# Kernel tuning notes

Hardware: AMD Instinct MI355X
Metric: run time of the kernel (lower is better)

The kernel has to match this reference:

```python
import jax, jax.numpy as jnp
import numpy as np

DIM = 1536
NH = 12
HD = 128
EPS = 1e-6


def _rope(x, freqs, f, h, w, start):
    # x: [B,S,N,D] with S == f*h*w; freqs: [1024, D//2, 2] (real, imag) unit rotations
    B, S, N, D = x.shape
    c = D // 2
    c0 = c - 2 * (c // 3)
    c1 = c // 3
    ff = jnp.broadcast_to(freqs[start:start + f, :c0][:, None, None], (f, h, w, c0, 2))
    fh = jnp.broadcast_to(freqs[:h, c0:c0 + c1][None, :, None], (f, h, w, c1, 2))
    fw = jnp.broadcast_to(freqs[:w, c0 + c1:c][None, None, :], (f, h, w, c1, 2))
    fr = jnp.concatenate([ff, fh, fw], axis=3).reshape(S, 1, c, 2)  # [S,1,c,2]
    xr, xi = x[..., 0::2], x[..., 1::2]          # interleaved real/imag pairs
    cr, ci = fr[None, ..., 0], fr[None, ..., 1]  # [1,S,1,c]
    yr = xr * cr - xi * ci
    yi = xr * ci + xi * cr
    return jnp.stack([yr, yi], axis=-1).reshape(B, S, N, D)


def _rms(x, g):
    return x * jax.lax.rsqrt(jnp.mean(x * x, axis=-1, keepdims=True) + EPS) * g


def setup_inputs():
    key = jax.random.key(0)
    ks = jax.random.split(key, 16)
    S = 3 * 30 * 52  # chunk_size = 3 frames * 1560 tokens/frame
    x = jax.random.normal(ks[0], (1, S, DIM), jnp.float32)
    fr = jax.random.normal(ks[1], (1024, HD // 2, 2), jnp.float32)
    fr = fr / jnp.sqrt(jnp.sum(fr * fr, axis=-1, keepdims=True) + 1e-12)  # unit-modulus rotations
    g_kmean = jax.random.uniform(ks[2], (1, NH, HD), jnp.float32)  # mean of relu(k): nonnegative
    g_kv = jax.random.normal(ks[3], (1, NH, HD, HD), jnp.float32) * 0.05
    p = lambda i, shp: jax.random.normal(ks[i], shp, jnp.float32) * 0.02
    return dict(
        x=x, freqs=fr, g_kmean=g_kmean, g_kv=g_kv,
        Wq=p(4, (DIM, DIM)), bq=p(5, (DIM,)),
        Wk=p(6, (DIM, DIM)), bk=p(7, (DIM,)),
        Wv=p(8, (DIM, DIM)), bv=p(9, (DIM,)),
        Wo=p(10, (DIM, DIM)), bo=p(11, (DIM,)),
        gq=jnp.ones((DIM,), jnp.float32), gk=jnp.ones((DIM,), jnp.float32),
        Wlin=p(12, (HD, HD)), blin=p(13, (HD,)),
        f_frames=3, h_grid=30, w_grid=52,
    )


def reference(x, freqs, g_kmean, g_kv, Wq, bq, Wk, bk, Wv, bv, Wo, bo, gq, gk, Wlin, blin, f_frames, h_grid, w_grid):
    B, S, _ = x.shape
    q = _rms(x @ Wq.T + bq, gq).reshape(B, S, NH, HD)
    k = _rms(x @ Wk.T + bk, gk).reshape(B, S, NH, HD)
    v = (x @ Wv.T + bv).reshape(B, S, NH, HD)
    rq = _rope(q, freqs, f_frames, h_grid, w_grid, 0)
    rk = _rope(k, freqs, f_frames, h_grid, w_grid, 0)
    # local window attention: at step 0 (current_start=0, empty cache, sink_size=0)
    # the working kv window is exactly the roped current chunk
    scores = jnp.einsum('bsnd,btnd->bnst', rq, rk) * (HD ** -0.5)
    x_local = jnp.einsum('bnst,btnd->bsnd', jax.nn.softmax(scores, axis=-1), v)
    # global linear-attention branch (kernel_func = relu feature map on q, roped q against kv state)
    qf = jax.nn.relu(q)
    z = 1.0 / (jnp.einsum('bsnd,bnd->bsn', qf, g_kmean) + 1e-6)
    xg = jnp.einsum('bsnd,bndm->bsnm', rq, g_kv) * z[..., None]
    xg = xg @ Wlin.T + blin
    out = (x_local + xg).reshape(B, S, DIM) @ Wo.T + bo
    return out
```

## Files before the change

kernel.cpp:

```cpp
#include <hip/hip_runtime.h>

typedef short s16x8 __attribute__((ext_vector_type(8)));
typedef float f32x4 __attribute__((ext_vector_type(4)));
typedef float f32x16 __attribute__((ext_vector_type(16)));
typedef unsigned short u16x4 __attribute__((ext_vector_type(4)));
typedef unsigned int u32x4 __attribute__((ext_vector_type(4)));

#define QSCALE (0.08838834764831845f * 1.4426950408889634f)

__device__ __forceinline__ unsigned short f2bf(float f) {
  unsigned int u = __float_as_uint(f);
  u += 0x7fffu + ((u >> 16) & 1u);
  return (unsigned short)(u >> 16);
}
__device__ __forceinline__ float bf2f(unsigned short h) {
  return __uint_as_float((unsigned int)h << 16);
}
__device__ __forceinline__ float fast_exp2(float x) {
  float r;
  asm("v_exp_f32 %0, %1" : "=v"(r) : "v"(x));
  return r;
}

__device__ __forceinline__ void gload16(const void* gp, void* lp) {
  __builtin_amdgcn_global_load_lds(
      (const __attribute__((address_space(1))) void*)gp,
      (__attribute__((address_space(3))) void*)lp,
      16, 0, 0);
}

__global__ void cast_f32_bf16_x4(const float* __restrict__ in,
                                 unsigned short* __restrict__ out, int n4) {
  int i = blockIdx.x * 256 + threadIdx.x;
  if (i >= n4) return;
  f32x4 v = *((const f32x4*)in + i);
  u16x4 o;
  o[0] = f2bf(v[0]); o[1] = f2bf(v[1]); o[2] = f2bf(v[2]); o[3] = f2bf(v[3]);
  *((u16x4*)out + i) = o;
}

__global__ void g2fill_kernel(const float* __restrict__ g_kv,
                              const float* __restrict__ Wlin,
                              unsigned short* __restrict__ G2c) {
  int h = blockIdx.x, m = blockIdx.y, d = threadIdx.x;
  const float* gk = g_kv + ((size_t)h * 128 + d) * 128;
  const float* wl = Wlin + (size_t)m * 128;
  float s = 0.f;
  for (int j = 0; j < 128; ++j) s += gk[j] * wl[j];
  G2c[((size_t)h * 128 + m) * 128 + d] = f2bf(s * (1.0f / QSCALE));
}

template <int MODE>
__global__ __launch_bounds__(256) void gemm_bt(
    const unsigned short* __restrict__ A, const unsigned short* __restrict__ B,
    const float* __restrict__ bias, void* __restrict__ Cout,
    int M, int N, int K, int lda, int ldb,
    const float* __restrict__ o0buf, const float* __restrict__ zbuf,
    const float* __restrict__ o1buf, const float* __restrict__ lbuf, int nsplit) {
  __shared__ __align__(16) unsigned short Asm_[128 * 64];
  __shared__ __align__(16) unsigned short Bsm_[128 * 64];
  const int tid = threadIdx.x;
  const int wid = tid >> 6, lane = tid & 63;
  const int mt = blockIdx.x, nt = blockIdx.y;
  const int wr = wid >> 1, wc = wid & 1;
  const int acol = (MODE == 3) ? nt * 128 : 0;
  f32x4 acc[4][4] = {};

  const int st_srccol = ((((lane & 7) << 4) ^ ((lane >> 3) << 4)) >> 1);
  const int st_rowoff = (lane >> 3);

  for (int k0 = 0; k0 < K; k0 += 64) {
    __syncthreads();
#pragma unroll
    for (int r = 0; r < 4; ++r) {
      int c = wid * 4 + r;
      int lrow = c * 8 + st_rowoff;
      int arow = mt * 128 + lrow; if (arow > M - 1) arow = M - 1;
      gload16(A + (size_t)arow * lda + acol + k0 + st_srccol,
              (char*)Asm_ + c * 1024 + lane * 16);
      int brow = nt * 128 + lrow;
      gload16(B + (size_t)brow * ldb + k0 + st_srccol,
              (char*)Bsm_ + c * 1024 + lane * 16);
    }
    __syncthreads();
#pragma unroll
    for (int kk = 0; kk < 2; ++kk) {
      int cb = (kk * 64 + ((lane >> 4) << 4)) ^ ((lane & 7) << 4);
      s16x8 af[4], bfr[4];
#pragma unroll
      for (int m = 0; m < 4; ++m)
        af[m] = *(const s16x8*)((const char*)Asm_ + (wr * 64 + m * 16 + (lane & 15)) * 128 + cb);
#pragma unroll
      for (int n = 0; n < 4; ++n)
        bfr[n] = *(const s16x8*)((const char*)Bsm_ + (wc * 64 + n * 16 + (lane & 15)) * 128 + cb);
#pragma unroll
      for (int m = 0; m < 4; ++m)
#pragma unroll
        for (int n = 0; n < 4; ++n)
          acc[m][n] = __builtin_amdgcn_mfma_f32_16x16x32_bf16(af[m], bfr[n], acc[m][n], 0, 0, 0);
    }
  }
  const int rb = mt * 128 + wr * 64, cbse = nt * 128 + wc * 64;
#pragma unroll
  for (int m = 0; m < 4; ++m) {
#pragma unroll
    for (int n = 0; n < 4; ++n) {
#pragma unroll
      for (int rg = 0; rg < 4; ++rg) {
        int rr = rb + m * 16 + ((lane >> 4) << 2) + rg;
        int cc = cbse + n * 16 + (lane & 15);
        if (rr < M) {
          float v = acc[m][n][rg];
          if (MODE == 0) {
            v += bias[cc];
            ((unsigned short*)Cout)[(size_t)rr * N + cc] = f2bf(v);
          } else if (MODE == 1) {
            v += bias[cc];
            ((float*)Cout)[(size_t)rr * N + cc] = v;
          } else {
            int hd = cc >> 7;
            float lsum = lbuf[(size_t)rr * 12 + hd];
            float osum = o0buf[(size_t)rr * N + cc];
            for (int s = 1; s < nsplit; ++s) {
              lsum += lbuf[((size_t)s * M + rr) * 12 + hd];
              osum += o1buf[(size_t)(s - 1) * M * 1536 + (size_t)rr * N + cc];
            }
            v = v * zbuf[(size_t)rr * 12 + hd] + osum * (1.0f / lsum) + bias[cc & 127];
            ((unsigned short*)Cout)[(size_t)rr * N + cc] = f2bf(v);
          }
        }
      }
    }
  }
}

__global__ __launch_bounds__(256) void rms_rope_kernel(
    const unsigned short* __restrict__ pre, const float* __restrict__ freqs,
    const float* __restrict__ g, const float* __restrict__ g_kmean,
    unsigned short* __restrict__ outr, float* __restrict__ zout,
    int S, int ld, float oscale,
    const int* __restrict__ hgp, const int* __restrict__ wgp) {
  const int s = blockIdx.x;
  const int tid = threadIdx.x;
  const int lane = tid & 63, wid = tid >> 6;
  const unsigned short* row = pre + (size_t)s * ld;
  unsigned int pv0, pv1, pv2;
  float ssq = 0.f;
  {
    pv0 = *(const unsigned int*)(row + 2 * (tid));
    pv1 = *(const unsigned int*)(row + 2 * (tid + 256));
    pv2 = *(const unsigned int*)(row + 2 * (tid + 512));
    float a0 = bf2f((unsigned short)(pv0 & 0xffffu)), b0 = bf2f((unsigned short)(pv0 >> 16));
    float a1 = bf2f((unsigned short)(pv1 & 0xffffu)), b1 = bf2f((unsigned short)(pv1 >> 16));
    float a2 = bf2f((unsigned short)(pv2 & 0xffffu)), b2 = bf2f((unsigned short)(pv2 >> 16));
    ssq = a0 * a0 + b0 * b0 + a1 * a1 + b1 * b1 + a2 * a2 + b2 * b2;
  }
#pragma unroll
  for (int m = 1; m < 64; m <<= 1) ssq += __shfl_xor(ssq, m, 64);
  __shared__ float wpart[4];
  if (lane == 0) wpart[wid] = ssq;
  __syncthreads();
  float tot = wpart[0] + wpart[1] + wpart[2] + wpart[3];
  float rms = rsqrtf(tot * (1.0f / 1536.0f) + 1e-6f);
  const int Wg = *wgp;
  const int HWg = (*hgp) * Wg;
  int fi = s / HWg; int rem = s - fi * HWg;
  int hi = rem / Wg; int wi = rem - hi * Wg;
  unsigned int pvs[3] = {pv0, pv1, pv2};
#pragma unroll
  for (int rd = 0; rd < 3; ++rd) {
    int p = tid + rd * 256;
    int c = p & 63;
    int fidx = (c < 22) ? fi : ((c < 43) ? hi : wi);
    float cr = freqs[fidx * 128 + 2 * c];
    float ci = freqs[fidx * 128 + 2 * c + 1];
    float xr = bf2f((unsigned short)(pvs[rd] & 0xffffu)) * rms * g[2 * p];
    float xi = bf2f((unsigned short)(pvs[rd] >> 16)) * rms * g[2 * p + 1];
    float yr = (xr * cr - xi * ci) * oscale;
    float yi = (xr * ci + xi * cr) * oscale;
    unsigned int ow = (unsigned int)f2bf(yr) | ((unsigned int)f2bf(yi) << 16);
    *(unsigned int*)(outr + (size_t)s * 1536 + 2 * p) = ow;
    if (zout != nullptr) {
      int head = p >> 6;
      float part = fmaxf(xr, 0.f) * g_kmean[head * 128 + 2 * c] +
                   fmaxf(xi, 0.f) * g_kmean[head * 128 + 2 * c + 1];
#pragma unroll
      for (int m = 1; m < 64; m <<= 1) part += __shfl_xor(part, m, 64);
      if (lane == 0) zout[(size_t)s * 12 + head] = 1.0f / (part + 1e-6f);
    }
  }
}

__global__ __launch_bounds__(256) void vtrans_kernel(const unsigned short* __restrict__ vpre,
                                                     unsigned short* __restrict__ vt, int S, int ld) {
  __shared__ unsigned short tile[64][66];
  int t0 = blockIdx.x * 64, c0 = blockIdx.y * 64;
  int tid = threadIdx.x;
#pragma unroll
  for (int rep = 0; rep < 16; ++rep) {
    int lin = rep * 256 + tid;
    int i = lin >> 6, j = lin & 63;
    int t = t0 + i; if (t > S - 1) t = S - 1;
    tile[i][j] = vpre[(size_t)t * ld + c0 + j];
  }
  __syncthreads();
#pragma unroll
  for (int rep = 0; rep < 16; ++rep) {
    int lin = rep * 256 + tid;
    int j = lin >> 6, i = lin & 63;
    int t = t0 + i;
    if (t < S) vt[(size_t)(c0 + j) * S + t] = tile[i][j];
  }
}

__global__ __launch_bounds__(256, 3) void attn_kernel(
    const unsigned short* __restrict__ rq, const unsigned short* __restrict__ rk,
    const unsigned short* __restrict__ vt, float* __restrict__ o0buf,
    float* __restrict__ o1buf, float* __restrict__ lbuf, int S, int nqb, int nsplit) {
  __shared__ __align__(16) unsigned short Ks[2][32 * 128];
  __shared__ __align__(16) unsigned short Vs[2][128 * 32];
  const int tid = threadIdx.x, wid = tid >> 6, lane = tid & 63;
  const int q32 = lane & 31, hi = lane >> 5;

  const int total = nqb * 12 * nsplit;
  int lg = blockIdx.x;
  if ((total & 7) == 0) lg = (lg & 7) * (total >> 3) + (lg >> 3);
  const int z = lg / (nqb * 12);
  int rem = lg - z * nqb * 12;
  const int h = rem / nqb;
  const int qb = rem - h * nqb;
  const int q0 = qb * 128 + wid * 32;

  const int seg = (((S + nsplit - 1) / nsplit) + 31) & ~31;
  const int tbeg = z * seg;
  const int tend = (tbeg + seg < S) ? (tbeg + seg) : S;
  float* obufz = (z == 0) ? o0buf : (o1buf + (size_t)(z - 1) * S * 1536);
  float* lbufz = lbuf + (size_t)z * S * 12;

  s16x8 qf[8];
  {
    int qrow = q0 + q32; if (qrow > S - 1) qrow = S - 1;
    const unsigned short* qp = rq + (size_t)qrow * 1536 + h * 128 + hi * 8;
#pragma unroll
    for (int dblk = 0; dblk < 8; ++dblk) qf[dblk] = *(const s16x8*)(qp + dblk * 16);
  }
  f32x16 o0 = {}, o1 = {}, o2 = {}, o3 = {};
  float lsum = 0.f;

  const int k_tok0 = tid >> 4;
  const int k_off = (tid & 15) * 16;
  const int v_d0 = tid >> 2;
  const int v_toff = (tid & 3) * 16;
  const int vswz = ((q32 >> 1) & 3) << 4;

#define STAGE(buf, t0s)                                                            \
  {                                                                                \
    _Pragma("unroll") for (int r = 0; r < 2; ++r) {                                \
      int ktok = k_tok0 + 16 * r;                                                  \
      int kb = k_off ^ ((ktok & 7) << 4);                                          \
      int trow = (t0s) + ktok; if (trow > S - 1) trow = S - 1;                     \
      gload16(rk + (size_t)trow * 1536 + h * 128 + (kb >> 1),                      \
              (char*)Ks[buf] + r * 4096 + tid * 16);                               \
      int dd = v_d0 + 64 * r;                                                      \
      int vb_ = v_toff ^ (((dd >> 1) & 3) << 4);                                   \
      int vtok = (t0s) + (vb_ >> 1); if (vtok > S - 8) vtok = S - 8;               \
      gload16(vt + (size_t)(h * 128 + dd) * S + vtok,                              \
              (char*)Vs[buf] + r * 4096 + tid * 16);                               \
    }                                                                              \
  }

  STAGE(0, tbeg);
  __syncthreads();
  int cur = 0;
  for (int t0 = tbeg; t0 < tend; t0 += 32) {
    if (t0 + 32 < tend) STAGE(cur ^ 1, t0 + 32);
    f32x16 sc = {};
    __builtin_amdgcn_s_setprio(1);
#pragma unroll
    for (int dblk = 0; dblk < 8; ++dblk) {
      s16x8 kfr = *(const s16x8*)((const char*)Ks[cur] + q32 * 256 +
                                  ((dblk * 32 + hi * 16) ^ ((q32 & 7) << 4)));
      sc = __builtin_amdgcn_mfma_f32_32x32x16_bf16(kfr, qf[dblk], sc, 0, 0, 0);
    }
    __builtin_amdgcn_s_setprio(0);
    const bool full = (t0 + 32 <= tend);
    unsigned int pk[8];
    float rs = 0.f;
#pragma unroll
    for (int j = 0; j < 8; ++j) {
      float p0, p1;
      if (full) {
        p0 = fast_exp2(sc[2 * j]);
        p1 = fast_exp2(sc[2 * j + 1]);
      } else {
        int r0 = 2 * j;
        int tk0 = t0 + (r0 & 3) + 8 * (r0 >> 2) + 4 * hi;
        p0 = (tk0 < tend) ? fast_exp2(sc[2 * j]) : 0.f;
        p1 = (tk0 + 1 < tend) ? fast_exp2(sc[2 * j + 1]) : 0.f;
      }
      unsigned int u0 = __float_as_uint(p0) & 0xffff0000u;
      unsigned int u1 = __float_as_uint(p1) & 0xffff0000u;
      rs += __uint_as_float(u0) + __uint_as_float(u1);
      pk[j] = (u0 >> 16) | u1;
    }
    lsum += rs;
    unsigned int x0 = pk[0], y0 = pk[2], x1 = pk[1], y1 = pk[3];
    asm("v_permlane32_swap_b32 %0, %1" : "+v"(x0), "+v"(y0));
    asm("v_permlane32_swap_b32 %0, %1" : "+v"(x1), "+v"(y1));
    unsigned int x2 = pk[4], y2 = pk[6], x3 = pk[5], y3 = pk[7];
    asm("v_permlane32_swap_b32 %0, %1" : "+v"(x2), "+v"(y2));
    asm("v_permlane32_swap_b32 %0, %1" : "+v"(x3), "+v"(y3));
    u32x4 pa0v = {x0, x1, y0, y1};
    u32x4 pa1v = {x2, x3, y2, y3};
    s16x8 pa0 = __builtin_bit_cast(s16x8, pa0v);
    s16x8 pa1 = __builtin_bit_cast(s16x8, pa1v);
    __builtin_amdgcn_s_setprio(1);
#pragma unroll
    for (int ks = 0; ks < 2; ++ks) {
      s16x8 pa = ks ? pa1 : pa0;
      const int tb = (ks * 32 + hi * 16) ^ vswz;
      const char* vbase = (const char*)Vs[cur] + q32 * 64 + tb;
      s16x8 vb;
      vb = *(const s16x8*)(vbase + 0 * 2048);
      o0 = __builtin_amdgcn_mfma_f32_32x32x16_bf16(pa, vb, o0, 0, 0, 0);
      vb = *(const s16x8*)(vbase + 1 * 2048);
      o1 = __builtin_amdgcn_mfma_f32_32x32x16_bf16(pa, vb, o1, 0, 0, 0);
      vb = *(const s16x8*)(vbase + 2 * 2048);
      o2 = __builtin_amdgcn_mfma_f32_32x32x16_bf16(pa, vb, o2, 0, 0, 0);
      vb = *(const s16x8*)(vbase + 3 * 2048);
      o3 = __builtin_amdgcn_mfma_f32_32x32x16_bf16(pa, vb, o3, 0, 0, 0);
    }
    __builtin_amdgcn_s_setprio(0);
    __syncthreads();
    cur ^= 1;
  }
  lsum += __shfl_xor(lsum, 32, 64);
  {
    int qrow = q0 + q32;
    if (hi == 0 && qrow < S) lbufz[(size_t)qrow * 12 + h] = lsum;
  }
#pragma unroll
  for (int r = 0; r < 16; ++r) {
    int qrow = q0 + (r & 3) + 8 * (r >> 2) + 4 * hi;
    if (qrow < S) {
      float* orow = obufz + (size_t)qrow * 1536 + h * 128 + q32;
      orow[0] = o0[r]; orow[32] = o1[r]; orow[64] = o2[r]; orow[96] = o3[r];
    }
  }
#undef STAGE
}

extern "C" void kernel_launch(void* const* d_in, const int* in_sizes, int n_in,
                              void* d_out, int out_size, void* d_ws, size_t ws_size,
                              hipStream_t stream) {
  const float* x = (const float*)d_in[0];
  const float* freqs = (const float*)d_in[1];
  const float* g_kmean = (const float*)d_in[2];
  const float* g_kv = (const float*)d_in[3];
  const float* Wq = (const float*)d_in[4];  const float* bq = (const float*)d_in[5];
  const float* Wk = (const float*)d_in[6];  const float* bk = (const float*)d_in[7];
  const float* Wv = (const float*)d_in[8];  const float* bv = (const float*)d_in[9];
  const float* Wo = (const float*)d_in[10]; const float* bo = (const float*)d_in[11];
  const float* gq = (const float*)d_in[12]; const float* gk = (const float*)d_in[13];
  const float* Wlin = (const float*)d_in[14]; const float* blin = (const float*)d_in[15];
  const int* hgp = (const int*)d_in[17];
  const int* wgp = (const int*)d_in[18];

  const int S = in_sizes[0] / 1536;

  char* ws = (char*)d_ws;
  const size_t SZ = (size_t)S * 1536 * 2;
  const size_t OSZ = (size_t)S * 1536 * 4;
  const size_t WSZ = (size_t)1536 * 1536 * 2;
  const size_t QKVSZ = (size_t)S * 4608 * 2;
  const size_t G2SZ = (size_t)12 * 128 * 128 * 2;
  size_t o_xbf = 0;
  size_t o_wqkv = o_xbf + SZ;
  size_t o_wo = o_wqkv + 3 * WSZ;
  size_t o_g2 = o_wo + WSZ;
  size_t o_qkv = o_g2 + G2SZ;
  size_t o_rk = o_qkv + QKVSZ;
  size_t o_vt = o_rk + SZ;
  size_t o_z = o_vt + SZ;
  size_t o_bqkv = o_z + (size_t)S * 12 * 4;
  size_t o_o1 = o_bqkv + 4608 * 4;

  int nsplit = 4;
  if (ws_size < o_o1 + (size_t)3 * OSZ + (size_t)4 * S * 12 * 4) nsplit = 2;
  size_t o_l = o_o1 + (size_t)(nsplit - 1) * OSZ;
  size_t need = o_l + (size_t)nsplit * S * 12 * 4;
  if (ws_size < need) return;

  unsigned short* xbf = (unsigned short*)(ws + o_xbf);
  unsigned short* wqkv = (unsigned short*)(ws + o_wqkv);
  unsigned short* wob = (unsigned short*)(ws + o_wo);
  unsigned short* g2c = (unsigned short*)(ws + o_g2);
  unsigned short* qkv = (unsigned short*)(ws + o_qkv);
  unsigned short* rkb = (unsigned short*)(ws + o_rk);
  unsigned short* vtb = (unsigned short*)(ws + o_vt);
  float* zbuf = (float*)(ws + o_z);
  float* bqkv = (float*)(ws + o_bqkv);
  unsigned short* rqb = xbf;
  float* o0buf = (float*)(ws + o_qkv);
  float* o1buf = (float*)(ws + o_o1);
  float* lbuf = (float*)(ws + o_l);
  unsigned short* ybf = (unsigned short*)(ws + o_qkv + OSZ);

  {
    int n4 = (S * 1536) / 4;
    cast_f32_bf16_x4<<<(n4 + 255) / 256, 256, 0, stream>>>(x, xbf, n4);
    int w4 = (1536 * 1536) / 4;
    int wg = (w4 + 255) / 256;
    cast_f32_bf16_x4<<<wg, 256, 0, stream>>>(Wq, wqkv, w4);
    cast_f32_bf16_x4<<<wg, 256, 0, stream>>>(Wk, wqkv + (size_t)1536 * 1536, w4);
    cast_f32_bf16_x4<<<wg, 256, 0, stream>>>(Wv, wqkv + (size_t)2 * 1536 * 1536, w4);
    cast_f32_bf16_x4<<<wg, 256, 0, stream>>>(Wo, wob, w4);
  }
  hipMemcpyAsync(bqkv, bq, 1536 * 4, hipMemcpyDeviceToDevice, stream);
  hipMemcpyAsync(bqkv + 1536, bk, 1536 * 4, hipMemcpyDeviceToDevice, stream);
  hipMemcpyAsync(bqkv + 3072, bv, 1536 * 4, hipMemcpyDeviceToDevice, stream);

  g2fill_kernel<<<dim3(12, 128), 128, 0, stream>>>(g_kv, Wlin, g2c);

  {
    dim3 ggrid((S + 127) / 128, 36);
    gemm_bt<0><<<ggrid, 256, 0, stream>>>(xbf, wqkv, bqkv, qkv, S, 4608, 1536, 1536, 1536,
                                          nullptr, nullptr, nullptr, nullptr, 0);
  }

  rms_rope_kernel<<<S, 256, 0, stream>>>(qkv, freqs, gq, g_kmean, rqb, zbuf, S, 4608, QSCALE, hgp, wgp);
  rms_rope_kernel<<<S, 256, 0, stream>>>(qkv + 1536, freqs, gk, nullptr, rkb, nullptr, S, 4608, 1.0f, hgp, wgp);

  vtrans_kernel<<<dim3((S + 63) / 64, 24), 256, 0, stream>>>(qkv + 3072, vtb, S, 4608);

  {
    int nqb = (S + 127) / 128;
    attn_kernel<<<dim3(nqb * 12 * nsplit), 256, 0, stream>>>(rqb, rkb, vtb,
                                                             o0buf, o1buf, lbuf, S, nqb, nsplit);
  }

  {
    dim3 ggrid((S + 127) / 128, 12);
    gemm_bt<3><<<ggrid, 256, 0, stream>>>(rqb, g2c, blin, ybf, S, 1536, 128, 1536, 128,
                                          o0buf, zbuf, o1buf, lbuf, nsplit);
    gemm_bt<1><<<ggrid, 256, 0, stream>>>(ybf, wob, bo, (float*)d_out, S, 1536, 1536, 1536, 1536,
                                          nullptr, nullptr, nullptr, nullptr, 0);
  }
}
```

Before: 464.5 us.

## Triple-buffer K/V staging in attention and fix KV split count to two

The attention kernel's K/V shared-memory staging goes from a double buffer to a ring of three, prefetching two tiles ahead. Each iteration now waits with explicit vmcnt counts and a raw s_barrier instead of __syncthreads, so one tile's loads can stay in flight across the barrier. The KV split count is also fixed at 2 instead of 4, which halves the partial-output buffers and combine work but gives fewer, longer blocks. Shared memory per block grows from 32 KB to 48 KB, which may lower occupancy relative to the launch bound of 3 blocks.

```diff
diff --git a/kernel.cpp b/kernel.cpp
--- a/kernel.cpp
+++ b/kernel.cpp
@@ -217,8 +217,8 @@
     const unsigned short* __restrict__ rq, const unsigned short* __restrict__ rk,
     const unsigned short* __restrict__ vt, float* __restrict__ o0buf,
     float* __restrict__ o1buf, float* __restrict__ lbuf, int S, int nqb, int nsplit) {
-  __shared__ __align__(16) unsigned short Ks[2][32 * 128];
-  __shared__ __align__(16) unsigned short Vs[2][128 * 32];
+  __shared__ __align__(16) unsigned short Ks[3 * 32 * 128];
+  __shared__ __align__(16) unsigned short Vs[3 * 32 * 128];
   const int tid = threadIdx.x, wid = tid >> 6, lane = tid & 63;
   const int q32 = lane & 31, hi = lane >> 5;
 
@@ -260,25 +260,38 @@
       int kb = k_off ^ ((ktok & 7) << 4);                                          \
       int trow = (t0s) + ktok; if (trow > S - 1) trow = S - 1;                     \
       gload16(rk + (size_t)trow * 1536 + h * 128 + (kb >> 1),                      \
-              (char*)Ks[buf] + r * 4096 + tid * 16);                               \
+              (char*)Ks + (buf) * 8192 + r * 4096 + tid * 16);                     \
       int dd = v_d0 + 64 * r;                                                      \
       int vb_ = v_toff ^ (((dd >> 1) & 3) << 4);                                   \
       int vtok = (t0s) + (vb_ >> 1); if (vtok > S - 8) vtok = S - 8;               \
       gload16(vt + (size_t)(h * 128 + dd) * S + vtok,                              \
-              (char*)Vs[buf] + r * 4096 + tid * 16);                               \
+              (char*)Vs + (buf) * 8192 + r * 4096 + tid * 16);                     \
     }                                                                              \
   }
 
   STAGE(0, tbeg);
-  __syncthreads();
+  if (tbeg + 32 < tend) {
+    STAGE(1, tbeg + 32);
+    asm volatile("s_waitcnt vmcnt(4)" ::: "memory");
+  } else {
+    asm volatile("s_waitcnt vmcnt(0)" ::: "memory");
+  }
+  __builtin_amdgcn_sched_barrier(0);
+  __builtin_amdgcn_s_barrier();
+  __builtin_amdgcn_sched_barrier(0);
+
   int cur = 0;
   for (int t0 = tbeg; t0 < tend; t0 += 32) {
-    if (t0 + 32 < tend) STAGE(cur ^ 1, t0 + 32);
+    const bool staged = (t0 + 64 < tend);
+    int stg = cur + 2; if (stg >= 3) stg -= 3;
+    if (staged) STAGE(stg, t0 + 64);
+    const char* Kc = (const char*)Ks + cur * 8192;
+    const char* Vc = (const char*)Vs + cur * 8192;
     f32x16 sc = {};
     __builtin_amdgcn_s_setprio(1);
 #pragma unroll
     for (int dblk = 0; dblk < 8; ++dblk) {
-      s16x8 kfr = *(const s16x8*)((const char*)Ks[cur] + q32 * 256 +
+      s16x8 kfr = *(const s16x8*)(Kc + q32 * 256 +
                                   ((dblk * 32 + hi * 16) ^ ((q32 & 7) << 4)));
       sc = __builtin_amdgcn_mfma_f32_32x32x16_bf16(kfr, qf[dblk], sc, 0, 0, 0);
     }
@@ -319,7 +332,7 @@
     for (int ks = 0; ks < 2; ++ks) {
       s16x8 pa = ks ? pa1 : pa0;
       const int tb = (ks * 32 + hi * 16) ^ vswz;
-      const char* vbase = (const char*)Vs[cur] + q32 * 64 + tb;
+      const char* vbase = Vc + q32 * 64 + tb;
       s16x8 vb;
       vb = *(const s16x8*)(vbase + 0 * 2048);
       o0 = __builtin_amdgcn_mfma_f32_32x32x16_bf16(pa, vb, o0, 0, 0, 0);
@@ -331,8 +344,15 @@
       o3 = __builtin_amdgcn_mfma_f32_32x32x16_bf16(pa, vb, o3, 0, 0, 0);
     }
     __builtin_amdgcn_s_setprio(0);
-    __syncthreads();
-    cur ^= 1;
+    if (staged) {
+      asm volatile("s_waitcnt vmcnt(4)" ::: "memory");
+    } else {
+      asm volatile("s_waitcnt vmcnt(0)" ::: "memory");
+    }
+    __builtin_amdgcn_sched_barrier(0);
+    __builtin_amdgcn_s_barrier();
+    __builtin_amdgcn_sched_barrier(0);
+    cur = cur + 1; if (cur >= 3) cur = 0;
   }
   lsum += __shfl_xor(lsum, 32, 64);
   {
@@ -367,6 +387,7 @@
   const int* wgp = (const int*)d_in[18];
 
   const int S = in_sizes[0] / 1536;
+  const int nsplit = 2;
 
   char* ws = (char*)d_ws;
   const size_t SZ = (size_t)S * 1536 * 2;
@@ -384,9 +405,6 @@
   size_t o_z = o_vt + SZ;
   size_t o_bqkv = o_z + (size_t)S * 12 * 4;
   size_t o_o1 = o_bqkv + 4608 * 4;
-
-  int nsplit = 4;
-  if (ws_size < o_o1 + (size_t)3 * OSZ + (size_t)4 * S * 12 * 4) nsplit = 2;
   size_t o_l = o_o1 + (size_t)(nsplit - 1) * OSZ;
   size_t need = o_l + (size_t)nsplit * S * 12 * 4;
   if (ws_size < need) return;
```

Result: no change. 461.7 us (-0.6%).

## Replace QKV GEMM with 256x256-tile double-buffered 8-wave kernel

Applied to the files above, without the earlier changes.

Adds a new bf16 GEMM kernel using 256x256 output tiles, 512 threads, double-buffered swizzled LDS staging interleaved with MFMA phases and setprio, and uses it for the fused QKV projection. The bigger tile raises data reuse per block and overlaps global loads with compute, cutting the global traffic and LDS stalls of the 128x128 kernel. It also pins the attention split count to 2 instead of choosing 4 when workspace allows, which changes attention occupancy and the number of partial buffers to combine. The grid for S=4680 holds only 19x18 blocks, so wave quantisation and the single-block-per-CU launch bound are risks.

```diff
diff --git a/kernel.cpp b/kernel.cpp
--- a/kernel.cpp
+++ b/kernel.cpp
@@ -48,6 +48,133 @@
   float s = 0.f;
   for (int j = 0; j < 128; ++j) s += gk[j] * wl[j];
   G2c[((size_t)h * 128 + m) * 128 + d] = f2bf(s * (1.0f / QSCALE));
+}
+
+__global__ __launch_bounds__(512, 1) void gemm256_bt(
+    const unsigned short* __restrict__ A, const unsigned short* __restrict__ B,
+    const float* __restrict__ bias, unsigned short* __restrict__ C,
+    int M, int N, int K) {
+  __shared__ __align__(16) unsigned short lds[2 * 2 * 2 * 128 * 64];
+  const int tid = threadIdx.x;
+  const int lane = tid & 63;
+  const int wid = tid >> 6;
+  const int wr = wid >> 2, wc = wid & 3;
+  const int mt = blockIdx.x, nt = blockIdx.y;
+
+  f32x4 acc[8][4] = {};
+
+  int st_row[2], st_col[2];
+#pragma unroll
+  for (int rep = 0; rep < 2; ++rep) {
+    int D = (rep * 512 + tid) * 16;
+    int L = D ^ (((D >> 9) & 1) << 5);
+    st_row[rep] = L >> 7;
+    st_col[rep] = (L & 127) >> 1;
+  }
+  const int NT = K / 64;
+
+#define G256_STAGE(mat, buf, half, kt)                                           \
+  {                                                                              \
+    const unsigned short* src_ = (mat) ? B : A;                                  \
+    int base_ = ((mat) ? nt : mt) * 256;                                         \
+    int lim_ = ((mat) ? N : M) - 1;                                              \
+    _Pragma("unroll") for (int rep = 0; rep < 2; ++rep) {                        \
+      int grow = base_ + (half) * 128 + st_row[rep];                             \
+      if (grow > lim_) grow = lim_;                                              \
+      gload16(src_ + (size_t)grow * K + (kt) * 64 + st_col[rep],                 \
+              (char*)lds + (((mat) * 2 + (buf)) * 2 + (half)) * 16384 +          \
+                  (rep * 512 + tid) * 16);                                       \
+    }                                                                            \
+  }
+
+  G256_STAGE(0, 0, 0, 0);
+  G256_STAGE(0, 0, 1, 0);
+  G256_STAGE(1, 0, 0, 0);
+  G256_STAGE(1, 0, 1, 0);
+  asm volatile("s_waitcnt vmcnt(0)" ::: "memory");
+  __builtin_amdgcn_sched_barrier(0);
+  __builtin_amdgcn_s_barrier();
+
+  const int swzkey = ((lane >> 2) & 1) << 5;
+  const int aRowB = lane & 15;
+  const int b0base = (lane >> 4) << 4;
+
+  s16x8 areg[4][2], breg[4][2];
+  const int NI = NT / 2;
+
+  for (int i = 0; i < NI; ++i) {
+#pragma unroll
+    for (int q = 0; q < 8; ++q) {
+      const int half_it = q >> 2;
+      const int buf = half_it;
+      const int mh = (q >> 1) & 1, nh = q & 1;
+      if (nh == 0) {
+#pragma unroll
+        for (int mm = 0; mm < 4; ++mm) {
+          int rowInHalf = (mh * 4 + mm) * 16 + aRowB;
+          const char* abase =
+              (const char*)lds + ((0 * 2 + buf) * 2 + wr) * 16384 + rowInHalf * 128;
+#pragma unroll
+          for (int kk = 0; kk < 2; ++kk)
+            areg[mm][kk] = *(const s16x8*)(abase + ((kk * 64 + b0base) ^ swzkey));
+        }
+      }
+      if (mh == 0) {
+#pragma unroll
+        for (int nn = 0; nn < 2; ++nn) {
+          int fn = nh * 2 + nn;
+          int rowInHalf = (wc & 1) * 64 + fn * 16 + aRowB;
+          const char* bbase =
+              (const char*)lds + ((1 * 2 + buf) * 2 + (wc >> 1)) * 16384 + rowInHalf * 128;
+#pragma unroll
+          for (int kk = 0; kk < 2; ++kk)
+            breg[fn][kk] = *(const s16x8*)(bbase + ((kk * 64 + b0base) ^ swzkey));
+        }
+      }
+      {
+        int tst = 2 * i + 1 + half_it;
+        if (tst < NT) {
+          int smat = (q & 3) >> 1;
+          int shalf = q & 1;
+          int sbuf = 1 - half_it;
+          G256_STAGE(smat, sbuf, shalf, tst);
+        }
+      }
+      __builtin_amdgcn_s_barrier();
+      asm volatile("s_waitcnt lgkmcnt(0)" ::: "memory");
+      __builtin_amdgcn_sched_barrier(0);
+      __builtin_amdgcn_s_setprio(1);
+#pragma unroll
+      for (int mm = 0; mm < 4; ++mm)
+#pragma unroll
+        for (int nn = 0; nn < 2; ++nn) {
+          const int fm = mh * 4 + mm, fn = nh * 2 + nn;
+          acc[fm][fn] = __builtin_amdgcn_mfma_f32_16x16x32_bf16(
+              areg[mm][0], breg[fn][0], acc[fm][fn], 0, 0, 0);
+          acc[fm][fn] = __builtin_amdgcn_mfma_f32_16x16x32_bf16(
+              areg[mm][1], breg[fn][1], acc[fm][fn], 0, 0, 0);
+        }
+      __builtin_amdgcn_s_setprio(0);
+      if ((q & 3) == 3) {
+        asm volatile("s_waitcnt vmcnt(0)" ::: "memory");
+      }
+      __builtin_amdgcn_sched_barrier(0);
+      __builtin_amdgcn_s_barrier();
+    }
+  }
+#pragma unroll
+  for (int fm = 0; fm < 8; ++fm) {
+#pragma unroll
+    for (int fn = 0; fn < 4; ++fn) {
+#pragma unroll
+      for (int rg = 0; rg < 4; ++rg) {
+        int rr = mt * 256 + wr * 128 + fm * 16 + ((lane >> 4) << 2) + rg;
+        int cc = nt * 256 + wc * 64 + fn * 16 + (lane & 15);
+        if (rr < M) C[(size_t)rr * N + cc] = f2bf(acc[fm][fn][rg] + bias[cc]);
+      }
+    }
+  }
+#undef G256_STAGE
 }
 
 template <int MODE>
@@ -111,10 +238,7 @@
         int cc = cbse + n * 16 + (lane & 15);
         if (rr < M) {
           float v = acc[m][n][rg];
-          if (MODE == 0) {
-            v += bias[cc];
-            ((unsigned short*)Cout)[(size_t)rr * N + cc] = f2bf(v);
-          } else if (MODE == 1) {
+          if (MODE == 1) {
             v += bias[cc];
             ((float*)Cout)[(size_t)rr * N + cc] = v;
           } else {
@@ -367,6 +491,7 @@
   const int* wgp = (const int*)d_in[18];
 
   const int S = in_sizes[0] / 1536;
+  const int nsplit = 2;
 
   char* ws = (char*)d_ws;
   const size_t SZ = (size_t)S * 1536 * 2;
@@ -384,9 +509,6 @@
   size_t o_z = o_vt + SZ;
   size_t o_bqkv = o_z + (size_t)S * 12 * 4;
   size_t o_o1 = o_bqkv + 4608 * 4;
-
-  int nsplit = 4;
-  if (ws_size < o_o1 + (size_t)3 * OSZ + (size_t)4 * S * 12 * 4) nsplit = 2;
   size_t o_l = o_o1 + (size_t)(nsplit - 1) * OSZ;
   size_t need = o_l + (size_t)nsplit * S * 12 * 4;
   if (ws_size < need) return;
@@ -423,9 +545,8 @@
   g2fill_kernel<<<dim3(12, 128), 128, 0, stream>>>(g_kv, Wlin, g2c);
 
   {
-    dim3 ggrid((S + 127) / 128, 36);
-    gemm_bt<0><<<ggrid, 256, 0, stream>>>(xbf, wqkv, bqkv, qkv, S, 4608, 1536, 1536, 1536,
-                                          nullptr, nullptr, nullptr, nullptr, 0);
+    dim3 ggrid((S + 255) / 256, 4608 / 256);
+    gemm256_bt<<<ggrid, 512, 0, stream>>>(xbf, wqkv, bqkv, qkv, S, 4608, 1536);
   }
 
   rms_rope_kernel<<<S, 256, 0, stream>>>(qkv, freqs, gq, g_kmean, rqb, zbuf, S, 4608, QSCALE, hgp, wgp);
```

Result: slower. 483.2 us (+4.0%).
